# Optimization experiments

Measured on AMD Instinct MI355X. Metric: run time of the kernel, lower is better.

## Reference

```python
import jax, jax.numpy as jnp
import numpy as np

NUM_SAMPLES = 4096
TAU = 0.07
EPS = 1e-20


def setup_inputs() -> dict:
    key = jax.random.key(0)
    flows = jax.random.normal(key, (32, 2, 512, 512), dtype=jnp.float32)
    return {"flows": flows}


def reference(flows):
    # flows: [b, 2, h, w]
    b, _, h, w = flows.shape
    hw = h * w
    # sampling weights: L2 norm over the 2 flow components, scaled by 1/tau
    dist = jnp.sqrt(jnp.sum(flows * flows, axis=1)) / TAU  # [b, h, w]
    dist = dist.reshape(b, hw)  # [b, h*w]
    # torch.multinomial(dist, k) without replacement == Gumbel-top-k on log-weights
    logits = jnp.log(dist + EPS)
    g = jax.random.gumbel(jax.random.key(42), (b, hw), dtype=flows.dtype)
    _, indices = jax.lax.top_k(logits + g, NUM_SAMPLES)  # [b, num_samples] int32
    # scatter-based mask (equivalent to one_hot(indices).max(dim=1), without the
    # huge [b, num_samples, h*w] intermediate)
    batch_idx = jnp.arange(b)[:, None]  # [b, 1]
    flat_masks = jnp.zeros((b, hw), dtype=flows.dtype).at[batch_idx, indices].set(1.0)
    masks = flat_masks.reshape(b, 1, h, w)  # [b, 1, h, w]
    sparse_output = masks * flows  # [b, 2, h, w]
    sparse_output = jnp.concatenate([sparse_output, masks], axis=1)  # [b, 3, h, w]
    return sparse_output, indices, masks
```

## Files before the change

### kernel.cpp

```cpp
#include <hip/hip_runtime.h>
#include <stdint.h>

#define HW 262144
#define NB 32
#define TOPK 4096
#define NTOTAL (NB * HW)
#define GBLK 4096
#define CBLK 32768

#define OUT_F4 8421376u
#define ZTHREADS 262144u

typedef float f32x4 __attribute__((ext_vector_type(4)));

#define OFF_WIN 33554432
#define OFF_HA  35651584
#define OFF_HB  37748736
#define OFF_STA 39845888
#define OFF_STT 39846144
#define OFF_FLG 39846272
#define OFF_CNT 39846400

__device__ __forceinline__ uint32_t rotl32(uint32_t x, int d) {
  return (x << d) | (x >> (32 - d));
}

__device__ __forceinline__ void threefry2x32_k42(uint32_t x0, uint32_t x1,
                                                 uint32_t& o0, uint32_t& o1) {
  const uint32_t ks0 = 0u;
  const uint32_t ks1 = 42u;
  const uint32_t ks2 = 0x1BD11BDAu ^ 0u ^ 42u;
  x0 += ks0;
  x1 += ks1;
#define TF_ROUND(r) { x0 += x1; x1 = rotl32(x1, (r)); x1 ^= x0; }
  TF_ROUND(13) TF_ROUND(15) TF_ROUND(26) TF_ROUND(6)
  x0 += ks1; x1 += ks2 + 1u;
  TF_ROUND(17) TF_ROUND(29) TF_ROUND(16) TF_ROUND(24)
  x0 += ks2; x1 += ks0 + 2u;
  TF_ROUND(13) TF_ROUND(15) TF_ROUND(26) TF_ROUND(6)
  x0 += ks0; x1 += ks1 + 3u;
  TF_ROUND(17) TF_ROUND(29) TF_ROUND(16) TF_ROUND(24)
  x0 += ks1; x1 += ks2 + 4u;
  TF_ROUND(13) TF_ROUND(15) TF_ROUND(26) TF_ROUND(6)
  x0 += ks2; x1 += ks0 + 5u;
#undef TF_ROUND
  o0 = x0;
  o1 = x1;
}

__device__ __forceinline__ float eigen_plogf(float xin) {
#pragma clang fp contract(off)
  uint32_t ux = __float_as_uint(xin);
  int e_int = (int)(ux >> 23) - 126;
  float x = __uint_as_float((ux & 0x007fffffu) | 0x3f000000u);
  float e = (float)e_int;
  const float SQRTHF = 0.707106781186547524f;
  bool m = (x < SQRTHF);
  float tmp = m ? x : 0.0f;
  x = x - 1.0f;
  e = e - (m ? 1.0f : 0.0f);
  x = x + tmp;
  float x2 = x * x;
  float x3 = x2 * x;
  float y  = fmaf(7.0376836292e-2f,  x, -1.1514610310e-1f);
  float y1 = fmaf(-1.2420140846e-1f, x,  1.4249322787e-1f);
  float y2 = fmaf(2.0000714765e-1f,  x, -2.4999993993e-1f);
  y  = fmaf(y,  x,  1.1676998740e-1f);
  y1 = fmaf(y1, x, -1.6668057665e-1f);
  y2 = fmaf(y2, x,  3.3333331174e-1f);
  y  = fmaf(y,  x3, y1);
  y  = fmaf(y,  x3, y2);
  y  = y * x3;
  float ey1 = e * -2.12194440e-4f;
  float t2  = x2 * 0.5f;
  y = y + ey1;
  x = x - t2;
  float ey2 = e * 0.693359375f;
  x = x + y;
  x = x + ey2;
  return x;
}

__device__ __forceinline__ float np_logf(float xin) {
#pragma clang fp contract(off)
  uint32_t ux = __float_as_uint(xin);
  int e2 = (int)(ux >> 23) - 127;
  float mant = __uint_as_float((ux & 0x007fffffu) | 0x3f800000u);
  if (mant >= 1.5f) { mant = mant * 0.5f; e2 += 1; }
  float e = (float)e2;
  float t = mant - 1.0f;
  float num = fmaf(2.589979117907922693523e-02f, t, 3.808837741388407920751e-01f);
  num = fmaf(num, t, 1.480000633400055983228e+00f);
  num = fmaf(num, t, 2.112677543073053063722e+00f);
  num = fmaf(num, t, 9.999999999999998702752e-01f);
  num = num * t;
  float den = fmaf(5.875095403124574342950e-03f, t, 1.546476374983906719538e-01f);
  den = fmaf(den, t, 9.864942958519418960339e-01f);
  den = fmaf(den, t, 2.453006071784736363091e+00f);
  den = fmaf(den, t, 2.612677543073109236779e+00f);
  den = fmaf(den, t, 1.0f);
  float r = num / den;
  return fmaf(e, 0.693147182464599609375f, r);
}

__device__ __forceinline__ uint32_t order_key(const float* __restrict__ flows,
                                              int p, uint32_t bits) {
#pragma clang fp contract(off)
  int b = p >> 18;
  int j = p & (HW - 1);
  const float* fb = flows + ((size_t)b << 19);
  float x = fb[j];
  float y = fb[j + HW];
  float xx = x * x;
  float yy = y * y;
  float ss = xx + yy;
  float sq = (float)sqrt((double)ss);
  float dist = (float)((double)sq / (double)0.07f);
  float logits = np_logf(dist + 1e-20f);
  float f = __uint_as_float((bits >> 9) | 0x3f800000u) - 1.0f;
  float u = fmaxf(f, 1.17549435e-38f);
  float g = -eigen_plogf(-eigen_plogf(u));
  float s = logits + g;
  uint32_t mm = __float_as_uint(s);
  mm = (mm & 0x80000000u) ? ~mm : (mm | 0x80000000u);
  return ~mm;
}

__global__ __launch_bounds__(1024) void k_compute(const float* __restrict__ flows,
                                                  uint32_t* __restrict__ d,
                                                  uint32_t* __restrict__ histA,
                                                  f32x4* __restrict__ outz) {
  __shared__ uint32_t lh[16384];
  for (int i = threadIdx.x; i < 16384; i += 1024) lh[i] = 0u;
  __syncthreads();
  int base = blockIdx.x * CBLK;
  int b = base >> 18;
  for (int it = 0; it < CBLK / 1024; ++it) {
    int p = base + it * 1024 + threadIdx.x;
    uint32_t o0, o1;
    threefry2x32_k42(0u, (uint32_t)p, o0, o1);
    uint32_t dv = order_key(flows, p, o0 ^ o1);
    d[p] = dv;
    atomicAdd(&lh[dv >> 18], 1u);
  }
  {
    const f32x4 z4 = (f32x4){0.f, 0.f, 0.f, 0.f};
    uint32_t tid = (uint32_t)blockIdx.x * 1024u + threadIdx.x;
    for (uint32_t i = tid; i < OUT_F4; i += ZTHREADS)
      __builtin_nontemporal_store(z4, &outz[i]);
  }
  __syncthreads();
  uint32_t* hb = histA + ((uint32_t)b << 14);
  for (int i = threadIdx.x; i < 16384; i += 1024) {
    uint32_t c = lh[i];
    if (c) atomicAdd(&hb[i], c);
  }
}

__global__ __launch_bounds__(1024) void k_scanA(const uint32_t* __restrict__ histA,
                                                uint32_t* __restrict__ stateA,
                                                uint32_t* __restrict__ stateT,
                                                uint32_t* __restrict__ flag) {
  int b = blockIdx.x;
  const uint32_t* h = histA + ((uint32_t)b << 14);
  int base = threadIdx.x * 16;
  uint32_t s = 0;
  for (int i = 0; i < 16; ++i) s += h[base + i];
  __shared__ uint32_t ls[1024];
  ls[threadIdx.x] = s;
  __syncthreads();
  for (int off = 1; off < 1024; off <<= 1) {
    uint32_t v = (threadIdx.x >= off) ? ls[threadIdx.x - off] : 0u;
    __syncthreads();
    ls[threadIdx.x] += v;
    __syncthreads();
  }
  uint32_t incl = ls[threadIdx.x];
  uint32_t excl = incl - s;
  if (excl < TOPK && TOPK <= incl) {
    uint32_t cum = excl;
    for (int i = 0; i < 16; ++i) {
      uint32_t c = h[base + i];
      if (cum + c >= TOPK) {
        uint32_t B = (uint32_t)(base + i);
        stateA[2 * b] = B;
        stateA[2 * b + 1] = TOPK - cum;
        stateT[b] = (B << 18) | 0x3FFFFu;
        flag[b] = (cum + c > 8192u) ? 1u : 0u;
        break;
      }
      cum += c;
    }
  }
}

__global__ __launch_bounds__(256) void k_histB(const uint32_t* __restrict__ d,
                                               const uint32_t* __restrict__ stateA,
                                               const uint32_t* __restrict__ flag,
                                               uint32_t* __restrict__ histB) {
  int base = blockIdx.x * GBLK;
  int b = base >> 18;
  if (flag[b] == 0u) return;
  uint32_t B = stateA[2 * b];
  for (int it = 0; it < GBLK / 256; ++it) {
    int p = base + it * 256 + threadIdx.x;
    uint32_t dv = d[p];
    if ((dv >> 18) == B)
      atomicAdd(&histB[((uint32_t)b << 14) + ((dv >> 4) & 0x3FFFu)], 1u);
  }
}

__global__ __launch_bounds__(1024) void k_scanB(const uint32_t* __restrict__ histB,
                                                const uint32_t* __restrict__ stateA,
                                                const uint32_t* __restrict__ flag,
                                                uint32_t* __restrict__ stateT) {
  int b = blockIdx.x;
  if (flag[b] == 0u) return;
  const uint32_t* h = histB + ((uint32_t)b << 14);
  uint32_t target = stateA[2 * b + 1];
  uint32_t B = stateA[2 * b];
  int base = threadIdx.x * 16;
  uint32_t s = 0;
  for (int i = 0; i < 16; ++i) s += h[base + i];
  __shared__ uint32_t ls[1024];
  ls[threadIdx.x] = s;
  __syncthreads();
  for (int off = 1; off < 1024; off <<= 1) {
    uint32_t v = (threadIdx.x >= off) ? ls[threadIdx.x - off] : 0u;
    __syncthreads();
    ls[threadIdx.x] += v;
    __syncthreads();
  }
  uint32_t incl = ls[threadIdx.x];
  uint32_t excl = incl - s;
  if (excl < target && target <= incl) {
    uint32_t cum = excl;
    for (int i = 0; i < 16; ++i) {
      uint32_t c = h[base + i];
      if (cum + c >= target) {
        stateT[b] = (B << 18) | ((uint32_t)(base + i) << 4) | 0xFu;
        break;
      }
      cum += c;
    }
  }
}

__global__ __launch_bounds__(256) void k_gather(const uint32_t* __restrict__ d,
                                                const uint32_t* __restrict__ stateT,
                                                uint32_t* __restrict__ cnt,
                                                unsigned long long* __restrict__ winners) {
  __shared__ unsigned long long buf[GBLK];
  __shared__ uint32_t lcnt;
  __shared__ uint32_t gbase;
  int base = blockIdx.x * GBLK;
  int b = base >> 18;
  uint32_t T = stateT[b];
  if (threadIdx.x == 0) lcnt = 0u;
  __syncthreads();
  for (int it = 0; it < GBLK / 256; ++it) {
    int p = base + it * 256 + threadIdx.x;
    uint32_t dv = d[p];
    if (dv <= T) {
      uint32_t pos = atomicAdd(&lcnt, 1u);
      buf[pos] = ((unsigned long long)dv << 32) |
                 (unsigned long long)(p & (HW - 1));
    }
  }
  __syncthreads();
  uint32_t n = lcnt;
  if (threadIdx.x == 0 && n) gbase = atomicAdd(&cnt[b], n);
  __syncthreads();
  for (uint32_t i = threadIdx.x; i < n; i += 256) {
    uint32_t pos = gbase + i;
    if (pos < 8192u) winners[(size_t)b * 8192 + pos] = buf[i];
  }
}

__global__ __launch_bounds__(256) void k_sort1(const uint32_t* __restrict__ cnt,
                                               unsigned long long* __restrict__ winners) {
  __shared__ unsigned long long s[1024];
  int blk = blockIdx.x;
  int b = blk >> 3;
  int c = blk & 7;
  uint32_t n = cnt[b];
  if (n > 8192u) n = 8192u;
  int goff = b * 8192 + c * 1024;
  for (int l = threadIdx.x; l < 1024; l += 256)
    s[l] = ((uint32_t)(c * 1024 + l) < n) ? winners[goff + l]
                                          : 0xFFFFFFFFFFFFFFFFull;
  __syncthreads();
  for (int k = 2; k <= 1024; k <<= 1) {
    for (int j = k >> 1; j > 0; j >>= 1) {
      for (int i = threadIdx.x; i < 1024; i += 256) {
        int ixj = i ^ j;
        if (ixj > i) {
          bool up = ((i & k) == 0);
          unsigned long long a = s[i];
          unsigned long long cc = s[ixj];
          if ((a > cc) == up) { s[i] = cc; s[ixj] = a; }
        }
      }
      __syncthreads();
    }
  }
  for (int l = threadIdx.x; l < 1024; l += 256) winners[goff + l] = s[l];
}

__global__ __launch_bounds__(1024) void k_rank(const unsigned long long* __restrict__ winners,
                                               const float* __restrict__ flows,
                                               float* __restrict__ out0,
                                               float* __restrict__ out_idx,
                                               float* __restrict__ out_masks) {
  __shared__ unsigned long long s[8192];
  int b = blockIdx.x;
  for (int i = threadIdx.x; i < 8192; i += 1024)
    s[i] = winners[(size_t)b * 8192 + i];
  __syncthreads();
  const float* fb = flows + ((size_t)b << 19);
  for (int i = threadIdx.x; i < 8192; i += 1024) {
    unsigned long long w = s[i];
    if (w == 0xFFFFFFFFFFFFFFFFull) continue;
    int rank = i & 1023;
    int myc = i >> 10;
    for (int c = 0; c < 8; ++c) {
      if (c == myc) continue;
      int lo = 0, hi = 1024;
      while (lo < hi) {
        int mid = (lo + hi) >> 1;
        if (s[(c << 10) + mid] < w) lo = mid + 1; else hi = mid;
      }
      rank += lo;
    }
    if (rank < TOPK) {
      uint32_t idx = (uint32_t)(w & 0xFFFFFFFFull);
      out_idx[(size_t)b * TOPK + rank] = (float)idx;
      float x = fb[idx];
      float y = fb[idx + HW];
      size_t o = ((size_t)b * 3) * HW + idx;
      out0[o] = x;
      out0[o + HW] = y;
      out0[o + 2 * HW] = 1.0f;
      out_masks[(size_t)b * HW + idx] = 1.0f;
    }
  }
}

extern "C" void kernel_launch(void* const* d_in, const int* in_sizes, int n_in,
                              void* d_out, int out_size, void* d_ws, size_t ws_size,
                              hipStream_t stream) {
  const float* flows = (const float*)d_in[0];
  float* out = (float*)d_out;
  char* ws = (char*)d_ws;

  uint32_t* d = (uint32_t*)ws;
  unsigned long long* winners = (unsigned long long*)(ws + OFF_WIN);
  uint32_t* histA = (uint32_t*)(ws + OFF_HA);
  uint32_t* histB = (uint32_t*)(ws + OFF_HB);
  uint32_t* stateA = (uint32_t*)(ws + OFF_STA);
  uint32_t* stateT = (uint32_t*)(ws + OFF_STT);
  uint32_t* flag = (uint32_t*)(ws + OFF_FLG);
  uint32_t* cnt = (uint32_t*)(ws + OFF_CNT);

  float* out_idx = out + (size_t)NB * 3 * HW;
  float* out_masks = out_idx + (size_t)NB * TOPK;

  (void)hipMemsetAsync(ws + OFF_HA, 0, 4194304 + 1024, stream);

  k_compute<<<NTOTAL / CBLK, 1024, 0, stream>>>(flows, d, histA, (f32x4*)out);
  k_scanA<<<NB, 1024, 0, stream>>>(histA, stateA, stateT, flag);
  k_histB<<<NTOTAL / GBLK, 256, 0, stream>>>(d, stateA, flag, histB);
  k_scanB<<<NB, 1024, 0, stream>>>(histB, stateA, flag, stateT);
  k_gather<<<NTOTAL / GBLK, 256, 0, stream>>>(d, stateT, cnt, winners);
  k_sort1<<<NB * 8, 256, 0, stream>>>(cnt, winners);
  k_rank<<<NB, 1024, 0, stream>>>(winners, flows, out, out_idx, out_masks);
}
```

Measured before the change: 364.4 us.

## Move output zeroing to dedicated blocks and fuse chunk sort into rank kernel

The output-zeroing loop moves out of the compute blocks into 64 extra blocks appended to k_compute's grid, and it now uses plain stores instead of nontemporal stores. The separate k_sort1 kernel is removed. Its bitonic sort of the eight 1024-element chunks now runs inside k_rank, one thread per element across all eight chunks. This saves one kernel launch and one global round-trip of the winners buffer. In exchange, the sort runs on only 32 blocks instead of 256, so there is less parallelism.

```diff
diff --git a/kernel.cpp b/kernel.cpp
--- a/kernel.cpp
+++ b/kernel.cpp
@@ -9,7 +9,8 @@
 #define CBLK 32768
 
 #define OUT_F4 8421376u
-#define ZTHREADS 262144u
+#define ZBLOCKS 64
+#define ZTHREADS (ZBLOCKS * 1024)
 
 typedef float f32x4 __attribute__((ext_vector_type(4)));
 
@@ -130,6 +131,13 @@
                                                   uint32_t* __restrict__ d,
                                                   uint32_t* __restrict__ histA,
                                                   f32x4* __restrict__ outz) {
+  if (blockIdx.x >= NTOTAL / CBLK) {
+    const f32x4 z4 = (f32x4){0.f, 0.f, 0.f, 0.f};
+    uint32_t tid = (uint32_t)(blockIdx.x - NTOTAL / CBLK) * 1024u + threadIdx.x;
+    for (uint32_t i = tid; i < OUT_F4; i += ZTHREADS)
+      outz[i] = z4;
+    return;
+  }
   __shared__ uint32_t lh[16384];
   for (int i = threadIdx.x; i < 16384; i += 1024) lh[i] = 0u;
   __syncthreads();
@@ -142,12 +150,6 @@
     uint32_t dv = order_key(flows, p, o0 ^ o1);
     d[p] = dv;
     atomicAdd(&lh[dv >> 18], 1u);
-  }
-  {
-    const f32x4 z4 = (f32x4){0.f, 0.f, 0.f, 0.f};
-    uint32_t tid = (uint32_t)blockIdx.x * 1024u + threadIdx.x;
-    for (uint32_t i = tid; i < OUT_F4; i += ZTHREADS)
-      __builtin_nontemporal_store(z4, &outz[i]);
   }
   __syncthreads();
   uint32_t* hb = histA + ((uint32_t)b << 14);
@@ -277,46 +279,38 @@
   }
 }
 
-__global__ __launch_bounds__(256) void k_sort1(const uint32_t* __restrict__ cnt,
-                                               unsigned long long* __restrict__ winners) {
-  __shared__ unsigned long long s[1024];
-  int blk = blockIdx.x;
-  int b = blk >> 3;
-  int c = blk & 7;
-  uint32_t n = cnt[b];
-  if (n > 8192u) n = 8192u;
-  int goff = b * 8192 + c * 1024;
-  for (int l = threadIdx.x; l < 1024; l += 256)
-    s[l] = ((uint32_t)(c * 1024 + l) < n) ? winners[goff + l]
-                                          : 0xFFFFFFFFFFFFFFFFull;
-  __syncthreads();
-  for (int k = 2; k <= 1024; k <<= 1) {
-    for (int j = k >> 1; j > 0; j >>= 1) {
-      for (int i = threadIdx.x; i < 1024; i += 256) {
-        int ixj = i ^ j;
-        if (ixj > i) {
-          bool up = ((i & k) == 0);
-          unsigned long long a = s[i];
-          unsigned long long cc = s[ixj];
-          if ((a > cc) == up) { s[i] = cc; s[ixj] = a; }
-        }
-      }
-      __syncthreads();
-    }
-  }
-  for (int l = threadIdx.x; l < 1024; l += 256) winners[goff + l] = s[l];
-}
-
 __global__ __launch_bounds__(1024) void k_rank(const unsigned long long* __restrict__ winners,
+                                               const uint32_t* __restrict__ cnt,
                                                const float* __restrict__ flows,
                                                float* __restrict__ out0,
                                                float* __restrict__ out_idx,
                                                float* __restrict__ out_masks) {
   __shared__ unsigned long long s[8192];
   int b = blockIdx.x;
+  uint32_t n = cnt[b];
+  if (n > 8192u) n = 8192u;
   for (int i = threadIdx.x; i < 8192; i += 1024)
-    s[i] = winners[(size_t)b * 8192 + i];
-  __syncthreads();
+    s[i] = ((uint32_t)i < n) ? winners[(size_t)b * 8192 + i]
+                             : 0xFFFFFFFFFFFFFFFFull;
+  __syncthreads();
+  {
+    int t = threadIdx.x;
+    for (int k = 2; k <= 1024; k <<= 1) {
+      for (int j = k >> 1; j > 0; j >>= 1) {
+        int ixj = t ^ j;
+        if (ixj > t) {
+          bool up = ((t & k) == 0);
+          for (int c = 0; c < 8; ++c) {
+            int base = c << 10;
+            unsigned long long a = s[base + t];
+            unsigned long long cc = s[base + ixj];
+            if ((a > cc) == up) { s[base + t] = cc; s[base + ixj] = a; }
+          }
+        }
+        __syncthreads();
+      }
+    }
+  }
   const float* fb = flows + ((size_t)b << 19);
   for (int i = threadIdx.x; i < 8192; i += 1024) {
     unsigned long long w = s[i];
@@ -367,11 +361,11 @@
 
   (void)hipMemsetAsync(ws + OFF_HA, 0, 4194304 + 1024, stream);
 
-  k_compute<<<NTOTAL / CBLK, 1024, 0, stream>>>(flows, d, histA, (f32x4*)out);
+  k_compute<<<NTOTAL / CBLK + ZBLOCKS, 1024, 0, stream>>>(flows, d, histA,
+                                                          (f32x4*)out);
   k_scanA<<<NB, 1024, 0, stream>>>(histA, stateA, stateT, flag);
   k_histB<<<NTOTAL / GBLK, 256, 0, stream>>>(d, stateA, flag, histB);
   k_scanB<<<NB, 1024, 0, stream>>>(histB, stateA, flag, stateT);
   k_gather<<<NTOTAL / GBLK, 256, 0, stream>>>(d, stateT, cnt, winners);
-  k_sort1<<<NB * 8, 256, 0, stream>>>(cnt, winners);
-  k_rank<<<NB, 1024, 0, stream>>>(winners, flows, out, out_idx, out_masks);
-}
+  k_rank<<<NB, 1024, 0, stream>>>(winners, cnt, flows, out, out_idx, out_masks);
+}
```

After: 369.5 us. Within noise of the previous version (+1.4%).
